# Optimization experiments

Hardware: AMD Instinct MI355X
Metric: run time of the kernel (lower is better)

The kernel has to match this reference:

```python
import jax, jax.numpy as jnp
import numpy as np

B, T, HID, OUT = 8, 256, 256, 6
DT = 0.1

def setup_inputs() -> dict:
    key = jax.random.key(0)
    ks = jax.random.split(key, 16)
    n = lambda i, shp, s: jax.random.normal(ks[i], shp, jnp.float32) * s
    return {
        "frames": jax.random.normal(ks[0], (B, T, 3, 64, 64), jnp.float32),
        "hidden_state": jnp.zeros((B, HID), jnp.float32),
        "conv1_w": n(1, (32, 3, 3, 3), 0.2), "conv1_b": jnp.zeros((32,), jnp.float32),
        "conv2_w": n(2, (64, 32, 3, 3), 0.1), "conv2_b": jnp.zeros((64,), jnp.float32),
        "conv3_w": n(3, (128, 64, 3, 3), 0.1), "conv3_b": jnp.zeros((128,), jnp.float32),
        "enc_w": n(4, (HID, 128), 0.08), "enc_b": jnp.zeros((HID,), jnp.float32),
        "ltc_wr": n(5, (HID, HID), 0.05), "ltc_wi": n(6, (HID, HID), 0.05),
        "ltc_b": jnp.zeros((HID,), jnp.float32),
        "ltc_tau": jax.random.uniform(ks[7], (HID,), jnp.float32, 0.5, 1.5),
        "ltc_a": n(8, (HID,), 1.0),
        "dec_w1": n(9, (128, HID), 0.08), "dec_b1": jnp.zeros((128,), jnp.float32),
        "dec_w2": n(10, (64, 128), 0.1), "dec_b2": jnp.zeros((64,), jnp.float32),
        "dec_w3": n(11, (OUT, 64), 0.1), "dec_b3": jnp.zeros((OUT,), jnp.float32),
    }

def _conv(x, w, b):
    y = jax.lax.conv_general_dilated(x, w, (2, 2), [(1, 1), (1, 1)],
                                     dimension_numbers=("NCHW", "OIHW", "NCHW"))
    return y + b[None, :, None, None]

def reference(frames, hidden_state, conv1_w, conv1_b, conv2_w, conv2_b, conv3_w, conv3_b,
              enc_w, enc_b, ltc_wr, ltc_wi, ltc_b, ltc_tau, ltc_a,
              dec_w1, dec_b1, dec_w2, dec_b2, dec_w3, dec_b3):
    Bb, Tt = frames.shape[:2]
    x = frames.reshape(Bb * Tt, 3, 64, 64)
    x = jax.nn.relu(_conv(x, conv1_w, conv1_b))   # (BT,32,32,32)
    x = jax.nn.relu(_conv(x, conv2_w, conv2_b))   # (BT,64,16,16)
    x = jax.nn.relu(_conv(x, conv3_w, conv3_b))   # (BT,128,8,8); adaptive pool to (8,8) is identity here
    feats = x.reshape(Bb, Tt, 128, 8, 8).transpose(0, 1, 3, 4, 2).reshape(Bb, Tt, 64, 128)
    node = feats @ enc_w.T + enc_b                # (B,T,64,HID)
    x_seq = node.mean(axis=2).transpose(1, 0, 2)  # (T,B,HID)

    def step(h, x_t):
        # LTC Euler update, dt=0.1, n_steps=1
        f = jnp.tanh(h @ ltc_wr.T + x_t @ ltc_wi.T + ltc_b)
        h_new = h + DT * (-(1.0 / ltc_tau + f) * h + f * ltc_a)
        y = jax.nn.relu(h_new @ dec_w1.T + dec_b1)
        y = jax.nn.relu(y @ dec_w2.T + dec_b2)
        c = y @ dec_w3.T + dec_b3
        return h_new, c

    final_hidden, controls = jax.lax.scan(step, hidden_state, x_seq)
    return controls.transpose(1, 0, 2), final_hidden
```

## Files before the change

### kernel.cpp

```cpp
#include <hip/hip_runtime.h>

#define T_STEPS 256
#define B_SZ 8
#define HID 256

typedef _Float16 hv2 __attribute__((ext_vector_type(2)));
typedef _Float16 f16x4 __attribute__((ext_vector_type(4)));
typedef float f32x4 __attribute__((ext_vector_type(4)));
typedef unsigned u32x4 __attribute__((ext_vector_type(4)));
union H2U { hv2 h; unsigned u; };
union U2F { uint2 u; f16x4 h; };
__device__ inline hv2 u2h(unsigned u){ H2U c; c.u = u; return c.h; }
__device__ inline unsigned h2u(hv2 h){ H2U c; c.h = h; return c.u; }
__device__ inline hv2 relu2(hv2 v){
  unsigned u = h2u(v);
  unsigned s = (u & 0x80008000u) >> 15;
  u &= ~(s * 0xFFFFu);
  return u2h(u);
}
__device__ inline unsigned packh2f(float lo, float hi){
  hv2 h; h.x = (_Float16)lo; h.y = (_Float16)hi; return h2u(h);
}

#define OFF_XW   0
#define OFF_HH   524288
#define OFF_WFT  1141760
#define OFF_BF   1174528
#define OFF_D1T  1174784
#define OFF_D2T  1207552
#define OFF_D3T  1215744
#define OFF_W1P  1216128
#define OFF_W2F  1216560
#define OFF_W3F  1225776
#define OFF_WRP  1262640

#define ENC_LDS_DW 16264

__global__ __launch_bounds__(256) void prep_kernel(
    const float* __restrict__ conv1_w, const float* __restrict__ conv2_w,
    const float* __restrict__ conv3_w, const float* __restrict__ enc_w,
    const float* __restrict__ enc_b,  const float* __restrict__ ltc_wi,
    const float* __restrict__ ltc_b,  const float* __restrict__ ltc_wr,
    const float* __restrict__ dec_w1,
    const float* __restrict__ dec_w2, const float* __restrict__ dec_w3,
    float* __restrict__ ws)
{
  int gtid = blockIdx.x * 256 + threadIdx.x;
  int nth = gridDim.x * 256;
  unsigned* wsu = (unsigned*)ws;
  for (int e = gtid; e < 128 * 256; e += nth) {
    int j = e >> 7, m = e & 127;
    float s = 0.f;
    for (int k = 0; k < 256; ++k) s = fmaf(ltc_wi[j*256 + k], enc_w[k*128 + m], s);
    ws[OFF_WFT + m*256 + j] = s;
  }
  for (int e = gtid; e < 256; e += nth) {
    float s = ltc_b[e];
    for (int k = 0; k < 256; ++k) s = fmaf(ltc_wi[e*256 + k], enc_b[k], s);
    ws[OFF_BF + e] = s;
  }
  for (int e = gtid; e < 27*16; e += nth) { int k = e>>4, p = e&15;
    wsu[OFF_W1P+e] = packh2f(conv1_w[(2*p)*27 + k], conv1_w[(2*p+1)*27 + k]); }
  for (int e = gtid; e < 9216; e += nth) {
    int dpair = e & 1;
    int nt = (e >> 1) & 3;
    int l  = (e >> 3) & 63;
    int g  = e >> 9;
    int kt = g % 9, hp = g / 9;
    int oc = nt*16 + (l & 15);
    int ic = hp*16 + ((l>>4)<<2) + (dpair<<1);
    int ky = kt/3, kx = kt%3;
    wsu[OFF_W2F + e] = packh2f(conv2_w[((oc*32 + ic)*3 + ky)*3 + kx],
                               conv2_w[((oc*32 + ic+1)*3 + ky)*3 + kx]);
  }
  for (int e = gtid; e < 36864; e += nth) {
    int dpair = e & 1;
    int tmp = e >> 1;
    int l = tmp & 63; tmp >>= 6;
    int nt = tmp & 7; tmp >>= 3;
    int kt = tmp;
    int kyx = kt >> 2;
    int ky = kyx/3, kx = kyx%3;
    int ic = ((kt & 3) << 4) + ((l>>4)<<2) + (dpair<<1);
    int oc = nt*16 + (l & 15);
    wsu[OFF_W3F + e] = packh2f(conv3_w[((oc*64 + ic)*3 + ky)*3 + kx],
                               conv3_w[((oc*64 + ic+1)*3 + ky)*3 + kx]);
  }
  for (int e = gtid; e < 32768; e += nth) {
    int i = e & 31;
    int j = (e >> 5) & 255;
    int q = e >> 13;
    wsu[OFF_WRP + e] = packh2f(ltc_wr[j*256 + q*64 + 2*i],
                               ltc_wr[j*256 + q*64 + 2*i + 1]);
  }
  for (int e = gtid; e < 256*128;e += nth) { int k = e>>7, i = e&127; ws[OFF_D1T+e] = dec_w1[i*256 + k]; }
  for (int e = gtid; e < 128*64; e += nth) { int k = e>>6, i = e&63;  ws[OFF_D2T+e] = dec_w2[i*128 + k]; }
  for (int e = gtid; e < 64*6;   e += nth) { int k = e/6,  o = e%6;   ws[OFF_D3T+e] = dec_w3[o*64 + k]; }
}

__global__ __launch_bounds__(256, 2) void enc_kernel(
    const float* __restrict__ frames,
    const float* __restrict__ b1, const float* __restrict__ b2,
    const float* __restrict__ b3, float* __restrict__ ws)
{
  extern __shared__ __align__(16) unsigned lds[];
  unsigned* buf0  = lds;
  unsigned* frH   = lds + 8192;
  unsigned* w3buf = lds + 8192;
  unsigned* w1s   = lds + 15320;
  float* fmp = (float*)(lds + 15752);
  _Float16* frHh = (_Float16*)frH;

  const int tid = threadIdx.x;
  const int l   = tid & 63;
  const int w   = tid >> 6;
  const int kg  = l >> 4;
  const int lc  = l & 15;
  const int bt  = blockIdx.x;
  const int b   = bt >> 8, t = bt & 255;
  const float* fr = frames + (size_t)bt * 12288;
  const unsigned* wsu = (const unsigned*)ws;
  const uint4* w2f4 = (const uint4*)(wsu + OFF_W2F);
  const uint4* w3src = (const uint4*)(wsu + OFF_W3F);

  {
    uint4 z4 = make_uint4(0u, 0u, 0u, 0u);
    for (int i = tid; i < 1782; i += 256) ((uint4*)frH)[i] = z4;
    if (tid < 216) ((uint2*)w1s)[tid] = ((const uint2*)(wsu + OFF_W1P))[tid];
  }
  __syncthreads();
  {
    const float4* fr4 = (const float4*)fr;
    #pragma unroll
    for (int p = 0; p < 12; ++p) {
      int fidx = p*256 + tid;
      float4 v = fr4[fidx];
      int ic = fidx >> 10, rem = fidx & 1023;
      int iy = rem >> 4, xq = rem & 15;
      int dw = ic*2376 + (iy+1)*36 + 2*xq + 2;
      uint2 pk;
      pk.x = packh2f(v.x, v.y);
      pk.y = packh2f(v.z, v.w);
      *(uint2*)(frH + dw) = pk;
    }
  }
  __syncthreads();

  f32x4 acc2[4][4];
  #pragma unroll
  for (int mi = 0; mi < 4; ++mi)
    #pragma unroll
    for (int nt = 0; nt < 4; ++nt) {
      float bb = b2[nt*16 + lc];
      acc2[mi][nt] = (f32x4){bb, bb, bb, bb};
    }

  for (int hp = 0; hp < 2; ++hp) {
    for (int p = 0; p < 4; ++p) {
      int pos = p*256 + tid;
      int y = pos >> 5, x = pos & 31;
      int base = 2*y*72 + 2*x;
      hv2 a1[8];
      #pragma unroll
      for (int o = 0; o < 8; ++o) { a1[o].x = (_Float16)b1[16*hp+2*o]; a1[o].y = (_Float16)b1[16*hp+2*o+1]; }
      #pragma unroll
      for (int ic = 0; ic < 3; ++ic)
        #pragma unroll
        for (int ky = 0; ky < 3; ++ky)
          #pragma unroll
          for (int kx = 0; kx < 3; ++kx) {
            _Float16 hf = frHh[base + ic*4752 + ky*72 + kx + 3];
            hv2 vs; vs.x = hf; vs.y = hf;
            int k = ic*9 + ky*3 + kx;
            uint4 wa = ((uint4*)w1s)[k*4 + hp*2];
            uint4 wb = ((uint4*)w1s)[k*4 + hp*2 + 1];
            a1[0] = vs * u2h(wa.x) + a1[0];
            a1[1] = vs * u2h(wa.y) + a1[1];
            a1[2] = vs * u2h(wa.z) + a1[2];
            a1[3] = vs * u2h(wa.w) + a1[3];
            a1[4] = vs * u2h(wb.x) + a1[4];
            a1[5] = vs * u2h(wb.y) + a1[5];
            a1[6] = vs * u2h(wb.z) + a1[6];
            a1[7] = vs * u2h(wb.w) + a1[7];
          }
      unsigned r0 = h2u(relu2(a1[0])), r1 = h2u(relu2(a1[1]));
      unsigned r2 = h2u(relu2(a1[2])), r3 = h2u(relu2(a1[3]));
      unsigned r4 = h2u(relu2(a1[4])), r5 = h2u(relu2(a1[5]));
      unsigned r6 = h2u(relu2(a1[6])), r7 = h2u(relu2(a1[7]));
      int s = pos & 3;
      uint4 v0, v1;
      if (s & 1) { v0 = make_uint4(r2,r3,r0,r1); v1 = make_uint4(r6,r7,r4,r5); }
      else       { v0 = make_uint4(r0,r1,r2,r3); v1 = make_uint4(r4,r5,r6,r7); }
      int sl = (s >> 1) & 1;
      ((uint4*)buf0)[pos*2 + sl]     = v0;
      ((uint4*)buf0)[pos*2 + (1^sl)] = v1;
    }
    __syncthreads();
    #pragma unroll
    for (int ky = 0; ky < 3; ++ky)
      #pragma unroll
      for (int kx = 0; kx < 3; ++kx) {
        int kt = ky*3 + kx;
        int bidx = ((hp*9 + kt)*64 + l)*2;
        uint4 q0 = w2f4[bidx];
        uint4 q1 = w2f4[bidx + 1];
        U2F bf[4];
        bf[0].u = make_uint2(q0.x, q0.y);
        bf[1].u = make_uint2(q0.z, q0.w);
        bf[2].u = make_uint2(q1.x, q1.y);
        bf[3].u = make_uint2(q1.z, q1.w);
        #pragma unroll
        for (int mi = 0; mi < 4; ++mi) {
          int mt = w*4 + mi;
          int iy = 2*mt - 1 + ky;
          if (iy >= 0) {
            int ix = 2*lc - 1 + kx;
            bool okx = (unsigned)ix < 32u;
            int pos1 = iy*32 + (okx ? ix : 0);
            U2F av; av.u = ((const uint2*)buf0)[pos1*4 + (kg ^ (pos1 & 3))];
            if (!okx) { av.u.x = 0u; av.u.y = 0u; }
            #pragma unroll
            for (int nt = 0; nt < 4; ++nt)
              acc2[mi][nt] = __builtin_amdgcn_mfma_f32_16x16x16f16(av.h, bf[nt].h, acc2[mi][nt], 0, 0, 0);
          }
        }
      }
    __syncthreads();
  }

  {
    uint4 s0a = w3src[tid];
    uint4 s0b = w3src[256 + tid];
    _Float16* act2h = (_Float16*)buf0;
    #pragma unroll
    for (int mi = 0; mi < 4; ++mi)
      #pragma unroll
      for (int nt = 0; nt < 4; ++nt)
        #pragma unroll
        for (int i = 0; i < 4; ++i) {
          int pos = (w*4 + mi)*16 + 4*kg + i;
          int oc = nt*16 + lc;
          float vv = fmaxf(acc2[mi][nt][i], 0.f);
          int ocp = (((oc >> 2) ^ (pos & 7)) << 2) + (oc & 3);
          act2h[pos*64 + ocp] = (_Float16)vv;
        }
    ((uint4*)w3buf)[tid] = s0a;
    ((uint4*)w3buf)[256 + tid] = s0b;
  }

  f32x4 acc3[8];
  #pragma unroll
  for (int nt = 0; nt < 8; ++nt) { float bb = b3[nt*16 + lc]; acc3[nt] = (f32x4){bb, bb, bb, bb}; }
  const int y3 = (w*16 + lc) >> 3, x3 = lc & 7;
  __syncthreads();

  for (int cc = 0; cc < 18; ++cc) {
    uint4 st0, st1;
    if (cc < 17) {
      st0 = w3src[(cc+1)*512 + tid];
      st1 = w3src[(cc+1)*512 + 256 + tid];
    }
    int kyx = cc >> 1;
    int ky = kyx / 3, kx = kyx % 3;
    int iy = 2*y3 - 1 + ky, ix = 2*x3 - 1 + kx;
    bool ok = ((unsigned)iy < 16u) && ((unsigned)ix < 16u);
    int posIn = (ok ? iy : 0)*16 + (ok ? ix : 0);
    int sw = posIn & 7;
    const uint2* bvp = (const uint2*)w3buf + (cc & 1)*1024;
    #pragma unroll
    for (int k2 = 0; k2 < 2; ++k2) {
      int kt = 2*cc + k2;
      int icb = (kt & 3)*4 + kg;
      U2F av; av.u = ((const uint2*)buf0)[posIn*16 + (icb ^ sw)];
      if (!ok) { av.u.x = 0u; av.u.y = 0u; }
      #pragma unroll
      for (int nt = 0; nt < 8; ++nt) {
        U2F bv; bv.u = bvp[((k2*8 + nt)<<6) + l];
        acc3[nt] = __builtin_amdgcn_mfma_f32_16x16x16f16(av.h, bv.h, acc3[nt], 0, 0, 0);
      }
    }
    if (cc < 17) {
      ((uint4*)w3buf)[((cc+1)&1)*512 + tid] = st0;
      ((uint4*)w3buf)[((cc+1)&1)*512 + 256 + tid] = st1;
    }
    __syncthreads();
  }

  #pragma unroll
  for (int nt = 0; nt < 8; ++nt) {
    float s = 0.f;
    #pragma unroll
    for (int i = 0; i < 4; ++i) s += fmaxf(acc3[nt][i], 0.f);
    s += __shfl_xor(s, 16);
    s += __shfl_xor(s, 32);
    if (l < 16) fmp[w*128 + nt*16 + l] = s;
  }
  __syncthreads();
  if (tid < 128) {
    float s = fmp[tid] + fmp[128 + tid] + fmp[256 + tid] + fmp[384 + tid];
    fmp[tid] = s * (1.f/64.f);
  }
  __syncthreads();
  {
    float accx = ws[OFF_BF + tid];
    const float* wfT = ws + OFF_WFT;
    for (int m = 0; m < 128; ++m) accx = fmaf(fmp[m], wfT[m*256 + tid], accx);
    ws[OFF_XW + (t*B_SZ + b)*HID + tid] = accx;
  }
}

__global__ __launch_bounds__(256, 1) void scan_kernel(
    const float* __restrict__ tau, const float* __restrict__ av,
    const float* __restrict__ h0,
    float* __restrict__ ws, float* __restrict__ outh)
{
  const int b = blockIdx.x;
  const int j = threadIdx.x;
  const int lane = j & 63;
  __shared__ unsigned hp16[2][128];
  __shared__ float hbuf[16*256];

  u32x4 wv[32];
  {
    const u32x4* wp = (const u32x4*)((const unsigned*)ws + OFF_WRP);
    #pragma unroll
    for (int r = 0; r < 32; ++r) {
      int q = r >> 3, rr = r & 7;
      wv[r] = wp[(q*256 + j)*8 + rr];
    }
  }
  const float tinv = 1.f / tau[j];
  const float aj = av[j];
  const float* xw = ws + OFF_XW;
  float* hh = ws + OFF_HH;

  float hreg = h0[b*256 + j];
  {
    float hnn = __shfl_xor(hreg, 1);
    if (!(j & 1)) hp16[0][j >> 1] = packh2f(hreg, hnn);
  }
  float xw_next = xw[(0*B_SZ + b)*HID + j];
  __syncthreads();

  for (int t = 0; t < T_STEPS; ++t) {
    float xwv = xw_next;
    xw_next = xw[((t+1)*B_SZ + b)*HID + j];
    uint2 vh = *((const uint2*)hp16[t & 1] + lane);
    hv2 a0 = {(_Float16)0.f, (_Float16)0.f};
    hv2 a1 = a0, a2 = a0, a3 = a0;
    #pragma unroll
    for (int r = 0; r < 32; ++r) {
      const int q = r >> 3, rr = r & 7;
      const int ln = (q << 4) + (rr << 1);
      u32x4 wq = wv[r];
      unsigned s0 = (unsigned)__builtin_amdgcn_readlane((int)vh.x, ln);
      unsigned s1 = (unsigned)__builtin_amdgcn_readlane((int)vh.y, ln);
      unsigned s2 = (unsigned)__builtin_amdgcn_readlane((int)vh.x, ln + 1);
      unsigned s3 = (unsigned)__builtin_amdgcn_readlane((int)vh.y, ln + 1);
      a0 = u2h(s0) * u2h(wq.x) + a0;
      a1 = u2h(s1) * u2h(wq.y) + a1;
      a2 = u2h(s2) * u2h(wq.z) + a2;
      a3 = u2h(s3) * u2h(wq.w) + a3;
    }
    hv2 s2v = (a0 + a1) + (a2 + a3);
    float pre = (float)s2v.x + (float)s2v.y + xwv;
    float f = 1.f - 2.f / (1.f + __expf(2.f * pre));
    float hn = fmaf(0.1f, fmaf(-(tinv + f), hreg, f * aj), hreg);
    float hnn = __shfl_xor(hn, 1);
    if (!(j & 1)) hp16[(t + 1) & 1][j >> 1] = packh2f(hn, hnn);
    hbuf[(t & 15)*256 + j] = hn;
    hreg = hn;
    if ((t & 15) == 15) {
      asm volatile("s_waitcnt lgkmcnt(0)" ::: "memory");
      __builtin_amdgcn_s_barrier();
      int base = t - 15;
      #pragma unroll
      for (int r = 0; r < 4; ++r) {
        int row = (j >> 6) + r*4;
        int col = (j & 63) << 2;
        *(float4*)(hh + ((base + row)*B_SZ + b)*HID + col) = *(float4*)(hbuf + row*256 + col);
      }
    }
    asm volatile("s_waitcnt lgkmcnt(0)" ::: "memory");
    __builtin_amdgcn_s_barrier();
  }
  outh[b*256 + j] = hreg;
}

__global__ __launch_bounds__(256) void dec_kernel(
    const float* __restrict__ db1, const float* __restrict__ db2,
    const float* __restrict__ db3, const float* __restrict__ ws,
    float* __restrict__ outc)
{
  const int bid = blockIdx.x;
  const int b = bid >> 8, t = bid & 255;
  const int tid = threadIdx.x;
  __shared__ float hloc[256];
  __shared__ float p1[2][128];
  __shared__ float y1s[128];
  __shared__ float p2[4][64];
  __shared__ float y2s[64];
  const float* hh  = ws + OFF_HH + (t*B_SZ + b)*HID;
  const float* d1T = ws + OFF_D1T;
  const float* d2T = ws + OFF_D2T;
  const float* d3T = ws + OFF_D3T;
  hloc[tid] = hh[tid];
  __syncthreads();
  {
    int i = tid & 127, hf = tid >> 7;
    float s = 0.f;
    for (int k = hf*128; k < hf*128 + 128; ++k) s = fmaf(hloc[k], d1T[k*128 + i], s);
    p1[hf][i] = s;
  }
  __syncthreads();
  if (tid < 128) y1s[tid] = fmaxf(p1[0][tid] + p1[1][tid] + db1[tid], 0.f);
  __syncthreads();
  {
    int i = tid & 63, r = tid >> 6;
    float s = 0.f;
    for (int k = r*32; k < r*32 + 32; ++k) s = fmaf(y1s[k], d2T[k*64 + i], s);
    p2[r][i] = s;
  }
  __syncthreads();
  if (tid < 64) y2s[tid] = fmaxf(p2[0][tid] + p2[1][tid] + p2[2][tid] + p2[3][tid] + db2[tid], 0.f);
  __syncthreads();
  if (tid < 6) {
    float s = db3[tid];
    for (int k = 0; k < 64; ++k) s = fmaf(y2s[k], d3T[k*6 + tid], s);
    outc[(b*T_STEPS + t)*6 + tid] = s;
  }
}

extern "C" void kernel_launch(void* const* d_in, const int* in_sizes, int n_in,
                              void* d_out, int out_size, void* d_ws, size_t ws_size,
                              hipStream_t stream)
{
  const float* frames = (const float*)d_in[0];
  const float* h0   = (const float*)d_in[1];
  const float* c1w  = (const float*)d_in[2];
  const float* c1b  = (const float*)d_in[3];
  const float* c2w  = (const float*)d_in[4];
  const float* c2b  = (const float*)d_in[5];
  const float* c3w  = (const float*)d_in[6];
  const float* c3b  = (const float*)d_in[7];
  const float* encw = (const float*)d_in[8];
  const float* encb = (const float*)d_in[9];
  const float* wr   = (const float*)d_in[10];
  const float* wi   = (const float*)d_in[11];
  const float* lb   = (const float*)d_in[12];
  const float* ltau = (const float*)d_in[13];
  const float* la   = (const float*)d_in[14];
  const float* dw1  = (const float*)d_in[15];
  const float* db1  = (const float*)d_in[16];
  const float* dw2  = (const float*)d_in[17];
  const float* db2  = (const float*)d_in[18];
  const float* dw3  = (const float*)d_in[19];
  const float* db3  = (const float*)d_in[20];
  float* out = (float*)d_out;
  float* ws  = (float*)d_ws;

  hipLaunchKernelGGL(prep_kernel, dim3(256), dim3(256), 0, stream,
                     c1w, c2w, c3w, encw, encb, wi, lb, wr, dw1, dw2, dw3, ws);
  hipLaunchKernelGGL(enc_kernel, dim3(2048), dim3(256), ENC_LDS_DW*4, stream,
                     frames, c1b, c2b, c3b, ws);
  hipLaunchKernelGGL(scan_kernel, dim3(B_SZ), dim3(256), 0, stream,
                     ltau, la, h0, ws, out + 12288);
  hipLaunchKernelGGL(dec_kernel, dim3(2048), dim3(256), 0, stream,
                     db1, db2, db3, ws, out);
}
```

Baseline: 417.7 us.

## Split scan recurrence matvec across four thread quarters with LDS partial-sum reduction

The serial LTC scan kernel now uses 1024 threads per batch row instead of 256. Each quarter of the block handles a quarter of the hidden-input dimension, holding 8 weight vectors in registers instead of 32, and writes a partial sum to shared memory. The first 256 threads reduce the partials and apply the update. The 16-step hbuf staging is replaced with a direct per-step global write of h. This shortens the per-step dependent FMA chain, but each step now needs a second barrier and an LDS reduction, which adds synchronization latency on the critical path.

```diff
diff --git a/kernel.cpp b/kernel.cpp
--- a/kernel.cpp
+++ b/kernel.cpp
@@ -309,82 +309,74 @@
   }
 }
 
-__global__ __launch_bounds__(256, 1) void scan_kernel(
+__global__ __launch_bounds__(1024, 1) void scan_kernel(
     const float* __restrict__ tau, const float* __restrict__ av,
     const float* __restrict__ h0,
     float* __restrict__ ws, float* __restrict__ outh)
 {
   const int b = blockIdx.x;
-  const int j = threadIdx.x;
-  const int lane = j & 63;
+  const int tid = threadIdx.x;
+  const int j = tid & 255;
+  const int q = tid >> 8;
+  const int lane = tid & 63;
   __shared__ unsigned hp16[2][128];
-  __shared__ float hbuf[16*256];
-
-  u32x4 wv[32];
-  {
-    const u32x4* wp = (const u32x4*)((const unsigned*)ws + OFF_WRP);
-    #pragma unroll
-    for (int r = 0; r < 32; ++r) {
-      int q = r >> 3, rr = r & 7;
-      wv[r] = wp[(q*256 + j)*8 + rr];
-    }
-  }
+  __shared__ float part[4][256];
+
+  const u32x4* wp = (const u32x4*)((const unsigned*)ws + OFF_WRP) + (q*256 + j)*8;
+  u32x4 w0 = wp[0], w1 = wp[1], w2 = wp[2], w3 = wp[3];
+  u32x4 w4 = wp[4], w5 = wp[5], w6 = wp[6], w7 = wp[7];
+  asm volatile("" : "+v"(w0), "+v"(w1), "+v"(w2), "+v"(w3),
+                    "+v"(w4), "+v"(w5), "+v"(w6), "+v"(w7));
+
   const float tinv = 1.f / tau[j];
   const float aj = av[j];
   const float* xw = ws + OFF_XW;
   float* hh = ws + OFF_HH;
 
-  float hreg = h0[b*256 + j];
-  {
+  float hreg = 0.f;
+  if (tid < 256) {
+    hreg = h0[b*256 + j];
     float hnn = __shfl_xor(hreg, 1);
     if (!(j & 1)) hp16[0][j >> 1] = packh2f(hreg, hnn);
   }
-  float xw_next = xw[(0*B_SZ + b)*HID + j];
+  float xw_next = (tid < 256) ? xw[(0*B_SZ + b)*HID + j] : 0.f;
   __syncthreads();
 
   for (int t = 0; t < T_STEPS; ++t) {
     float xwv = xw_next;
-    xw_next = xw[((t+1)*B_SZ + b)*HID + j];
-    uint2 vh = *((const uint2*)hp16[t & 1] + lane);
+    if (tid < 256) xw_next = xw[((t+1)*B_SZ + b)*HID + j];
+    uint2 vh = *((const uint2*)hp16[t & 1] + (q*16 + (lane & 15)));
     hv2 a0 = {(_Float16)0.f, (_Float16)0.f};
     hv2 a1 = a0, a2 = a0, a3 = a0;
-    #pragma unroll
-    for (int r = 0; r < 32; ++r) {
-      const int q = r >> 3, rr = r & 7;
-      const int ln = (q << 4) + (rr << 1);
-      u32x4 wq = wv[r];
-      unsigned s0 = (unsigned)__builtin_amdgcn_readlane((int)vh.x, ln);
-      unsigned s1 = (unsigned)__builtin_amdgcn_readlane((int)vh.y, ln);
-      unsigned s2 = (unsigned)__builtin_amdgcn_readlane((int)vh.x, ln + 1);
-      unsigned s3 = (unsigned)__builtin_amdgcn_readlane((int)vh.y, ln + 1);
-      a0 = u2h(s0) * u2h(wq.x) + a0;
-      a1 = u2h(s1) * u2h(wq.y) + a1;
-      a2 = u2h(s2) * u2h(wq.z) + a2;
-      a3 = u2h(s3) * u2h(wq.w) + a3;
-    }
+    #define SCAN_R(wq, r) { \
+      unsigned s0 = (unsigned)__builtin_amdgcn_readlane((int)vh.x, 2*(r)); \
+      unsigned s1 = (unsigned)__builtin_amdgcn_readlane((int)vh.y, 2*(r)); \
+      unsigned s2 = (unsigned)__builtin_amdgcn_readlane((int)vh.x, 2*(r)+1); \
+      unsigned s3 = (unsigned)__builtin_amdgcn_readlane((int)vh.y, 2*(r)+1); \
+      a0 = u2h(s0) * u2h((wq).x) + a0; \
+      a1 = u2h(s1) * u2h((wq).y) + a1; \
+      a2 = u2h(s2) * u2h((wq).z) + a2; \
+      a3 = u2h(s3) * u2h((wq).w) + a3; }
+    SCAN_R(w0, 0) SCAN_R(w1, 1) SCAN_R(w2, 2) SCAN_R(w3, 3)
+    SCAN_R(w4, 4) SCAN_R(w5, 5) SCAN_R(w6, 6) SCAN_R(w7, 7)
+    #undef SCAN_R
     hv2 s2v = (a0 + a1) + (a2 + a3);
-    float pre = (float)s2v.x + (float)s2v.y + xwv;
-    float f = 1.f - 2.f / (1.f + __expf(2.f * pre));
-    float hn = fmaf(0.1f, fmaf(-(tinv + f), hreg, f * aj), hreg);
-    float hnn = __shfl_xor(hn, 1);
-    if (!(j & 1)) hp16[(t + 1) & 1][j >> 1] = packh2f(hn, hnn);
-    hbuf[(t & 15)*256 + j] = hn;
-    hreg = hn;
-    if ((t & 15) == 15) {
-      asm volatile("s_waitcnt lgkmcnt(0)" ::: "memory");
-      __builtin_amdgcn_s_barrier();
-      int base = t - 15;
-      #pragma unroll
-      for (int r = 0; r < 4; ++r) {
-        int row = (j >> 6) + r*4;
-        int col = (j & 63) << 2;
-        *(float4*)(hh + ((base + row)*B_SZ + b)*HID + col) = *(float4*)(hbuf + row*256 + col);
-      }
-    }
+    part[q][j] = (float)s2v.x + (float)s2v.y;
     asm volatile("s_waitcnt lgkmcnt(0)" ::: "memory");
     __builtin_amdgcn_s_barrier();
-  }
-  outh[b*256 + j] = hreg;
+    if (tid < 256) {
+      float pre = part[0][j] + part[1][j] + part[2][j] + part[3][j] + xwv;
+      float f = 1.f - 2.f / (1.f + __expf(2.f * pre));
+      float hn = fmaf(0.1f, fmaf(-(tinv + f), hreg, f * aj), hreg);
+      hh[(t*B_SZ + b)*HID + j] = hn;
+      float hnn = __shfl_xor(hn, 1);
+      if (!(j & 1)) hp16[(t + 1) & 1][j >> 1] = packh2f(hn, hnn);
+      hreg = hn;
+    }
+    asm volatile("s_waitcnt lgkmcnt(0)" ::: "memory");
+    __builtin_amdgcn_s_barrier();
+  }
+  if (tid < 256) outh[b*256 + j] = hreg;
 }
 
 __global__ __launch_bounds__(256) void dec_kernel(
@@ -463,7 +455,7 @@
                      c1w, c2w, c3w, encw, encb, wi, lb, wr, dw1, dw2, dw3, ws);
   hipLaunchKernelGGL(enc_kernel, dim3(2048), dim3(256), ENC_LDS_DW*4, stream,
                      frames, c1b, c2b, c3b, ws);
-  hipLaunchKernelGGL(scan_kernel, dim3(B_SZ), dim3(256), 0, stream,
+  hipLaunchKernelGGL(scan_kernel, dim3(B_SZ), dim3(1024), 0, stream,
                      ltau, la, h0, ws, out + 12288);
   hipLaunchKernelGGL(dec_kernel, dim3(2048), dim3(256), 0, stream,
                      db1, db2, db3, ws, out);
```

Result: slower. 430.2 us (+3.0%).

## Fuse encoder and LTC scan into one kernel with per-timestep counters

Applied to the files above, without the earlier changes.

Merges the encoder and recurrent scan kernels into one launch. The first 8 blocks run the scan for each batch element, while the remaining blocks encode frames in timestep-major order. Each encoder block bumps a per-timestep atomic counter after writing its input projection, and the scan blocks spin on that counter before consuming step t. This overlaps the serial scan with encoding instead of waiting for the whole encoder to finish. It relies on the scan blocks being co-resident with the encoder blocks to avoid deadlock, and the scan blocks now run under the encoder's launch bounds and LDS footprint.

```diff
diff --git a/kernel.cpp b/kernel.cpp
--- a/kernel.cpp
+++ b/kernel.cpp
@@ -33,6 +33,7 @@
 #define OFF_W2F  1216560
 #define OFF_W3F  1225776
 #define OFF_WRP  1262640
+#define OFF_CNT  1295408
 
 #define ENC_LDS_DW 16264
 
@@ -48,6 +49,7 @@
   int gtid = blockIdx.x * 256 + threadIdx.x;
   int nth = gridDim.x * 256;
   unsigned* wsu = (unsigned*)ws;
+  for (int e = gtid; e < 256; e += nth) wsu[OFF_CNT + e] = 0u;
   for (int e = gtid; e < 128 * 256; e += nth) {
     int j = e >> 7, m = e & 127;
     float s = 0.f;
@@ -98,12 +100,126 @@
   for (int e = gtid; e < 64*6;   e += nth) { int k = e/6,  o = e%6;   ws[OFF_D3T+e] = dec_w3[o*64 + k]; }
 }
 
-__global__ __launch_bounds__(256, 2) void enc_kernel(
+__global__ __launch_bounds__(256, 2) void fused_kernel(
     const float* __restrict__ frames,
     const float* __restrict__ b1, const float* __restrict__ b2,
-    const float* __restrict__ b3, float* __restrict__ ws)
+    const float* __restrict__ b3,
+    const float* __restrict__ tau, const float* __restrict__ av,
+    const float* __restrict__ h0, float* __restrict__ outh,
+    float* __restrict__ ws)
 {
   extern __shared__ __align__(16) unsigned lds[];
+  const int tid = threadIdx.x;
+  unsigned* cnt = (unsigned*)ws + OFF_CNT;
+
+  if (blockIdx.x < 8) {
+    const int b = blockIdx.x;
+    const int j = tid;
+    const int lane = tid & 63;
+    unsigned* hp16 = lds;
+    float* hbuf = (float*)(lds + 256);
+
+    u32x4 wv[32];
+    {
+      const u32x4* wp = (const u32x4*)((const unsigned*)ws + OFF_WRP);
+      #pragma unroll
+      for (int r = 0; r < 32; ++r) {
+        int q = r >> 3, rr = r & 7;
+        wv[r] = wp[(q*256 + j)*8 + rr];
+      }
+    }
+    const float tinv = 1.f / tau[j];
+    const float aj = av[j];
+    const float* xw = ws + OFF_XW;
+    float* hh = ws + OFF_HH;
+
+    float hreg = h0[b*256 + j];
+    {
+      float hnn = __shfl_xor(hreg, 1);
+      if (!(j & 1)) hp16[j >> 1] = packh2f(hreg, hnn);
+    }
+    __syncthreads();
+
+    bool pre_ok = false;
+    float xw_pref = 0.f;
+    for (int t = 0; t < T_STEPS; ++t) {
+      float xwv;
+      if (!pre_ok) {
+        unsigned c;
+        do {
+          unsigned cl = 0;
+          if (lane == 0)
+            cl = __hip_atomic_load(cnt + t, __ATOMIC_RELAXED, __HIP_MEMORY_SCOPE_AGENT);
+          c = (unsigned)__builtin_amdgcn_readfirstlane((int)cl);
+          if (c < 8) __builtin_amdgcn_s_sleep(16);
+        } while (c < 8);
+        __builtin_amdgcn_fence(__ATOMIC_ACQUIRE, "agent");
+        xwv = xw[(t*B_SZ + b)*HID + j];
+      } else {
+        xwv = xw_pref;
+      }
+      pre_ok = false;
+      if (t + 1 < T_STEPS) {
+        unsigned cl = 0;
+        if (lane == 0)
+          cl = __hip_atomic_load(cnt + t + 1, __ATOMIC_RELAXED, __HIP_MEMORY_SCOPE_AGENT);
+        unsigned c = (unsigned)__builtin_amdgcn_readfirstlane((int)cl);
+        if (c >= 8) {
+          __builtin_amdgcn_fence(__ATOMIC_ACQUIRE, "agent");
+          xw_pref = xw[((t+1)*B_SZ + b)*HID + j];
+          pre_ok = true;
+        }
+      }
+      uint2 vh = *((const uint2*)(hp16 + (t & 1)*128) + lane);
+      hv2 a0 = {(_Float16)0.f, (_Float16)0.f};
+      hv2 a1 = a0, a2 = a0, a3 = a0;
+      #define SCAN_R(r) { \
+        const int q = (r) >> 3, rr = (r) & 7; \
+        const int ln = (q << 4) + (rr << 1); \
+        u32x4 wq = wv[r]; \
+        unsigned s0 = (unsigned)__builtin_amdgcn_readlane((int)vh.x, ln); \
+        unsigned s1 = (unsigned)__builtin_amdgcn_readlane((int)vh.y, ln); \
+        unsigned s2 = (unsigned)__builtin_amdgcn_readlane((int)vh.x, ln + 1); \
+        unsigned s3 = (unsigned)__builtin_amdgcn_readlane((int)vh.y, ln + 1); \
+        a0 = u2h(s0) * u2h(wq.x) + a0; \
+        a1 = u2h(s1) * u2h(wq.y) + a1; \
+        a2 = u2h(s2) * u2h(wq.z) + a2; \
+        a3 = u2h(s3) * u2h(wq.w) + a3; }
+      SCAN_R(0)  SCAN_R(1)  SCAN_R(2)  SCAN_R(3)
+      SCAN_R(4)  SCAN_R(5)  SCAN_R(6)  SCAN_R(7)
+      SCAN_R(8)  SCAN_R(9)  SCAN_R(10) SCAN_R(11)
+      SCAN_R(12) SCAN_R(13) SCAN_R(14) SCAN_R(15)
+      SCAN_R(16) SCAN_R(17) SCAN_R(18) SCAN_R(19)
+      SCAN_R(20) SCAN_R(21) SCAN_R(22) SCAN_R(23)
+      SCAN_R(24) SCAN_R(25) SCAN_R(26) SCAN_R(27)
+      SCAN_R(28) SCAN_R(29) SCAN_R(30) SCAN_R(31)
+      #undef SCAN_R
+      hv2 s2v = (a0 + a1) + (a2 + a3);
+      float pre = (float)s2v.x + (float)s2v.y + xwv;
+      float f = 1.f - 2.f / (1.f + __expf(2.f * pre));
+      float hn = fmaf(0.1f, fmaf(-(tinv + f), hreg, f * aj), hreg);
+      float hnn = __shfl_xor(hn, 1);
+      if (!(j & 1)) hp16[((t + 1) & 1)*128 + (j >> 1)] = packh2f(hn, hnn);
+      hbuf[(t & 15)*256 + j] = hn;
+      hreg = hn;
+      if ((t & 15) == 15) {
+        asm volatile("s_waitcnt lgkmcnt(0)" ::: "memory");
+        __builtin_amdgcn_s_barrier();
+        int base = t - 15;
+        #pragma unroll
+        for (int r = 0; r < 4; ++r) {
+          int row = (j >> 6) + r*4;
+          int col = (j & 63) << 2;
+          *(float4*)(hh + ((base + row)*B_SZ + b)*HID + col) = *(float4*)(hbuf + row*256 + col);
+        }
+      }
+      asm volatile("s_waitcnt lgkmcnt(0)" ::: "memory");
+      __builtin_amdgcn_s_barrier();
+    }
+    outh[b*256 + j] = hreg;
+    return;
+  }
+
   unsigned* buf0  = lds;
   unsigned* frH   = lds + 8192;
   unsigned* w3buf = lds + 8192;
@@ -111,14 +227,14 @@
   float* fmp = (float*)(lds + 15752);
   _Float16* frHh = (_Float16*)frH;
 
-  const int tid = threadIdx.x;
   const int l   = tid & 63;
   const int w   = tid >> 6;
   const int kg  = l >> 4;
   const int lc  = l & 15;
-  const int bt  = blockIdx.x;
-  const int b   = bt >> 8, t = bt & 255;
-  const float* fr = frames + (size_t)bt * 12288;
+  const int bt  = blockIdx.x - 8;
+  const int t   = bt >> 3;
+  const int b   = bt & 7;
+  const float* fr = frames + (size_t)(b*256 + t) * 12288;
   const unsigned* wsu = (const unsigned*)ws;
   const uint4* w2f4 = (const uint4*)(wsu + OFF_W2F);
   const uint4* w3src = (const uint4*)(wsu + OFF_W3F);
@@ -217,11 +333,11 @@
             int ix = 2*lc - 1 + kx;
             bool okx = (unsigned)ix < 32u;
             int pos1 = iy*32 + (okx ? ix : 0);
-            U2F av; av.u = ((const uint2*)buf0)[pos1*4 + (kg ^ (pos1 & 3))];
-            if (!okx) { av.u.x = 0u; av.u.y = 0u; }
+            U2F av2; av2.u = ((const uint2*)buf0)[pos1*4 + (kg ^ (pos1 & 3))];
+            if (!okx) { av2.u.x = 0u; av2.u.y = 0u; }
             #pragma unroll
             for (int nt = 0; nt < 4; ++nt)
-              acc2[mi][nt] = __builtin_amdgcn_mfma_f32_16x16x16f16(av.h, bf[nt].h, acc2[mi][nt], 0, 0, 0);
+              acc2[mi][nt] = __builtin_amdgcn_mfma_f32_16x16x16f16(av2.h, bf[nt].h, acc2[mi][nt], 0, 0, 0);
           }
         }
       }
@@ -271,12 +387,12 @@
     for (int k2 = 0; k2 < 2; ++k2) {
       int kt = 2*cc + k2;
       int icb = (kt & 3)*4 + kg;
-      U2F av; av.u = ((const uint2*)buf0)[posIn*16 + (icb ^ sw)];
-      if (!ok) { av.u.x = 0u; av.u.y = 0u; }
+      U2F av2; av2.u = ((const uint2*)buf0)[posIn*16 + (icb ^ sw)];
+      if (!ok) { av2.u.x = 0u; av2.u.y = 0u; }
       #pragma unroll
       for (int nt = 0; nt < 8; ++nt) {
         U2F bv; bv.u = bvp[((k2*8 + nt)<<6) + l];
-        acc3[nt] = __builtin_amdgcn_mfma_f32_16x16x16f16(av.h, bv.h, acc3[nt], 0, 0, 0);
+        acc3[nt] = __builtin_amdgcn_mfma_f32_16x16x16f16(av2.h, bv.h, acc3[nt], 0, 0, 0);
       }
     }
     if (cc < 17) {
@@ -307,84 +423,11 @@
     for (int m = 0; m < 128; ++m) accx = fmaf(fmp[m], wfT[m*256 + tid], accx);
     ws[OFF_XW + (t*B_SZ + b)*HID + tid] = accx;
   }
-}
-
-__global__ __launch_bounds__(256, 1) void scan_kernel(
-    const float* __restrict__ tau, const float* __restrict__ av,
-    const float* __restrict__ h0,
-    float* __restrict__ ws, float* __restrict__ outh)
-{
-  const int b = blockIdx.x;
-  const int j = threadIdx.x;
-  const int lane = j & 63;
-  __shared__ unsigned hp16[2][128];
-  __shared__ float hbuf[16*256];
-
-  u32x4 wv[32];
-  {
-    const u32x4* wp = (const u32x4*)((const unsigned*)ws + OFF_WRP);
-    #pragma unroll
-    for (int r = 0; r < 32; ++r) {
-      int q = r >> 3, rr = r & 7;
-      wv[r] = wp[(q*256 + j)*8 + rr];
-    }
-  }
-  const float tinv = 1.f / tau[j];
-  const float aj = av[j];
-  const float* xw = ws + OFF_XW;
-  float* hh = ws + OFF_HH;
-
-  float hreg = h0[b*256 + j];
-  {
-    float hnn = __shfl_xor(hreg, 1);
-    if (!(j & 1)) hp16[0][j >> 1] = packh2f(hreg, hnn);
-  }
-  float xw_next = xw[(0*B_SZ + b)*HID + j];
-  __syncthreads();
-
-  for (int t = 0; t < T_STEPS; ++t) {
-    float xwv = xw_next;
-    xw_next = xw[((t+1)*B_SZ + b)*HID + j];
-    uint2 vh = *((const uint2*)hp16[t & 1] + lane);
-    hv2 a0 = {(_Float16)0.f, (_Float16)0.f};
-    hv2 a1 = a0, a2 = a0, a3 = a0;
-    #pragma unroll
-    for (int r = 0; r < 32; ++r) {
-      const int q = r >> 3, rr = r & 7;
-      const int ln = (q << 4) + (rr << 1);
-      u32x4 wq = wv[r];
-      unsigned s0 = (unsigned)__builtin_amdgcn_readlane((int)vh.x, ln);
-      unsigned s1 = (unsigned)__builtin_amdgcn_readlane((int)vh.y, ln);
-      unsigned s2 = (unsigned)__builtin_amdgcn_readlane((int)vh.x, ln + 1);
-      unsigned s3 = (unsigned)__builtin_amdgcn_readlane((int)vh.y, ln + 1);
-      a0 = u2h(s0) * u2h(wq.x) + a0;
-      a1 = u2h(s1) * u2h(wq.y) + a1;
-      a2 = u2h(s2) * u2h(wq.z) + a2;
-      a3 = u2h(s3) * u2h(wq.w) + a3;
-    }
-    hv2 s2v = (a0 + a1) + (a2 + a3);
-    float pre = (float)s2v.x + (float)s2v.y + xwv;
-    float f = 1.f - 2.f / (1.f + __expf(2.f * pre));
-    float hn = fmaf(0.1f, fmaf(-(tinv + f), hreg, f * aj), hreg);
-    float hnn = __shfl_xor(hn, 1);
-    if (!(j & 1)) hp16[(t + 1) & 1][j >> 1] = packh2f(hn, hnn);
-    hbuf[(t & 15)*256 + j] = hn;
-    hreg = hn;
-    if ((t & 15) == 15) {
-      asm volatile("s_waitcnt lgkmcnt(0)" ::: "memory");
-      __builtin_amdgcn_s_barrier();
-      int base = t - 15;
-      #pragma unroll
-      for (int r = 0; r < 4; ++r) {
-        int row = (j >> 6) + r*4;
-        int col = (j & 63) << 2;
-        *(float4*)(hh + ((base + row)*B_SZ + b)*HID + col) = *(float4*)(hbuf + row*256 + col);
-      }
-    }
-    asm volatile("s_waitcnt lgkmcnt(0)" ::: "memory");
-    __builtin_amdgcn_s_barrier();
-  }
-  outh[b*256 + j] = hreg;
+  __syncthreads();
+  if (tid == 0) {
+    __threadfence();
+    atomicAdd(cnt + t, 1u);
+  }
 }
 
 __global__ __launch_bounds__(256) void dec_kernel(
@@ -461,10 +504,8 @@
 
   hipLaunchKernelGGL(prep_kernel, dim3(256), dim3(256), 0, stream,
                      c1w, c2w, c3w, encw, encb, wi, lb, wr, dw1, dw2, dw3, ws);
-  hipLaunchKernelGGL(enc_kernel, dim3(2048), dim3(256), ENC_LDS_DW*4, stream,
-                     frames, c1b, c2b, c3b, ws);
-  hipLaunchKernelGGL(scan_kernel, dim3(B_SZ), dim3(256), 0, stream,
-                     ltau, la, h0, ws, out + 12288);
+  hipLaunchKernelGGL(fused_kernel, dim3(2056), dim3(256), ENC_LDS_DW*4, stream,
+                     frames, c1b, c2b, c3b, ltau, la, h0, out + 12288, ws);
   hipLaunchKernelGGL(dec_kernel, dim3(2048), dim3(256), 0, stream,
                      db1, db2, db3, ws, out);
 }
```

Measured after the change: 417.9 us. No clear change (+0.1%).
